# Performance work log

Measured on AMD Instinct MI355X. Metric: run time of the kernel, lower is better.

Reference implementation:

```python
import jax, jax.numpy as jnp
import numpy as np

B, S, D, N, MAX_W = 8, 512, 768, 512, 16  # batch, seq_len, input_dim, num_spans, max span width
TINY = 1e-13  # tiny_value_of_dtype(float32)


def setup_inputs() -> dict:
    key = jax.random.key(0)
    k1, k2, k3, k4 = jax.random.split(key, 4)
    sequence_tensor = jax.random.normal(k1, (B, S, D), dtype=jnp.float32)
    starts = jax.random.randint(k2, (B, N), 0, S - MAX_W)
    widths = jax.random.randint(k3, (B, N), 0, MAX_W)  # inclusive width-1 in [0, MAX_W-1]
    span_indices = jnp.stack([starts, starts + widths], axis=-1)  # (B, N, 2), end inclusive
    att_w = jax.random.normal(k4, (D,), dtype=jnp.float32) / np.sqrt(D)
    att_b = jnp.zeros((1,), dtype=jnp.float32)
    return {"sequence_tensor": sequence_tensor, "span_indices": span_indices,
            "att_w": att_w, "att_b": att_b}


def reference(sequence_tensor, span_indices, att_w, att_b):
    # global attention logits: Linear(D, 1) over every token  -> (B, S)
    logits = jnp.einsum('bsd,d->bs', sequence_tensor, att_w) + att_b[0]

    starts = span_indices[..., 0]                      # (B, N)
    ends = span_indices[..., 1]                        # (B, N), inclusive
    widths = ends - starts                             # (B, N)

    # batched_span_select: MAX_W is the (static) max span width
    rng = jnp.arange(MAX_W)                            # (W,)
    span_mask = rng[None, None, :] <= widths[..., None]          # (B, N, W)
    raw_idx = starts[..., None] + rng[None, None, :]             # (B, N, W)
    span_mask = span_mask & (raw_idx < S) & (raw_idx >= 0)
    idx = raw_idx * span_mask                                    # zeroed where masked

    b_idx = jnp.arange(sequence_tensor.shape[0])[:, None, None]
    span_emb = sequence_tensor[b_idx, idx]             # (B, N, W, D) gather
    span_logits = logits[b_idx[..., 0].reshape(-1, 1, 1), idx] if False else logits[b_idx, idx]  # (B, N, W)

    # masked_softmax (memory_efficient=False): softmax(vector*mask) * mask, renormalized
    maskf = span_mask.astype(span_logits.dtype)
    attn = jax.nn.softmax(span_logits * maskf, axis=-1) * maskf
    attn = attn / (attn.sum(axis=-1, keepdims=True) + TINY)

    # weighted sum over span width -> (B, N, D)
    return jnp.einsum('bnw,bnwd->bnd', attn, span_emb)
```

## Files before the change

### kernel.cpp

```cpp
#include <hip/hip_runtime.h>
#include <hip/hip_bf16.h>

#define B 8
#define S 512
#define D 768
#define N 512
#define MAX_W 16

__global__ __launch_bounds__(256) void logits_kernel(
    const float* __restrict__ seq,
    const float* __restrict__ att_w,
    const float* __restrict__ att_b,
    float* __restrict__ logits)
{
    const int wave = threadIdx.x >> 6;
    const int lane = threadIdx.x & 63;
    const int row  = blockIdx.x * 4 + wave;

    const float4* seq4 = (const float4*)(seq + (size_t)row * D);
    const float4* w4   = (const float4*)att_w;

    float acc = 0.0f;
#pragma unroll
    for (int i = 0; i < 3; ++i) {
        float4 a = seq4[lane + 64 * i];
        float4 w = w4[lane + 64 * i];
        acc += a.x * w.x + a.y * w.y + a.z * w.z + a.w * w.w;
    }
#pragma unroll
    for (int off = 32; off > 0; off >>= 1)
        acc += __shfl_xor(acc, off, 64);

    if (lane == 0) logits[row] = acc + att_b[0];
}

__global__ __launch_bounds__(192) void span_kernel(
    const float* __restrict__ seq,
    const int*   __restrict__ spans,
    const float* __restrict__ logits,
    float* __restrict__ out)
{
    const int span  = blockIdx.x;
    const int b     = span >> 9;
    const int start = spans[span * 2 + 0];
    const int end   = spans[span * 2 + 1];
    const int width = end - start;

    const float* lrow = logits + b * S + start;
    float wgt[MAX_W];
    float m = -1e30f;
#pragma unroll
    for (int i = 0; i < MAX_W; ++i) {
        float l = lrow[i];
        wgt[i] = l;
        if (i <= width) m = fmaxf(m, l);
    }
    float sum = 0.0f;
#pragma unroll
    for (int i = 0; i < MAX_W; ++i) {
        float e = (i <= width) ? __expf(wgt[i] - m) : 0.0f;
        wgt[i] = e;
        sum += e;
    }
    const float inv = 1.0f / sum;

    const float4* seqb = (const float4*)(seq + ((size_t)b * S + start) * D);
    const int tid = threadIdx.x;
    float4 acc = make_float4(0.f, 0.f, 0.f, 0.f);
#pragma unroll
    for (int i = 0; i < MAX_W; ++i) {
        if (i <= width) {
            float4 v = seqb[i * (D / 4) + tid];
            float w = wgt[i];
            acc.x += w * v.x;
            acc.y += w * v.y;
            acc.z += w * v.z;
            acc.w += w * v.w;
        }
    }
    acc.x *= inv; acc.y *= inv; acc.z *= inv; acc.w *= inv;

    float4* out4 = (float4*)(out + (size_t)span * D);
    out4[tid] = acc;
}

extern "C" void kernel_launch(void* const* d_in, const int* in_sizes, int n_in,
                              void* d_out, int out_size, void* d_ws, size_t ws_size,
                              hipStream_t stream) {
    const float* seq    = (const float*)d_in[0];
    const int*   spans  = (const int*)d_in[1];
    const float* att_w  = (const float*)d_in[2];
    const float* att_b  = (const float*)d_in[3];
    float* out = (float*)d_out;
    float* logits = (float*)d_ws;

    logits_kernel<<<(B * S) / 4, 256, 0, stream>>>(seq, att_w, att_b, logits);

    span_kernel<<<B * N, 192, 0, stream>>>(seq, spans, logits, out);
}
```

Before: 84.65 us.

## Fuse attention logit computation into span kernel and reorder block-to-span mapping

Removes the separate logits kernel: each span block computes the dot products of its gathered rows with att_w, reduces them through LDS, then does the softmax and the weighted sum from rows held in registers. This avoids a launch and a full pass over the sequence tensor, at the cost of redundant dot products for overlapping spans and extra syncs. Blocks are also remapped so that consecutive block IDs stride across batches. The bias is dropped because softmax is shift-invariant.

```diff
diff --git a/kernel.cpp b/kernel.cpp
--- a/kernel.cpp
+++ b/kernel.cpp
@@ -6,95 +6,108 @@
 #define D 768
 #define N 512
 #define MAX_W 16
+#define BLOCK 192
+#define ROW_F 196
 
-__global__ __launch_bounds__(256) void logits_kernel(
+__global__ __launch_bounds__(BLOCK) void fused_span_kernel(
     const float* __restrict__ seq,
+    const int2*  __restrict__ spans,
     const float* __restrict__ att_w,
-    const float* __restrict__ att_b,
-    float* __restrict__ logits)
-{
-    const int wave = threadIdx.x >> 6;
-    const int lane = threadIdx.x & 63;
-    const int row  = blockIdx.x * 4 + wave;
-
-    const float4* seq4 = (const float4*)(seq + (size_t)row * D);
-    const float4* w4   = (const float4*)att_w;
-
-    float acc = 0.0f;
-#pragma unroll
-    for (int i = 0; i < 3; ++i) {
-        float4 a = seq4[lane + 64 * i];
-        float4 w = w4[lane + 64 * i];
-        acc += a.x * w.x + a.y * w.y + a.z * w.z + a.w * w.w;
-    }
-#pragma unroll
-    for (int off = 32; off > 0; off >>= 1)
-        acc += __shfl_xor(acc, off, 64);
-
-    if (lane == 0) logits[row] = acc + att_b[0];
-}
-
-__global__ __launch_bounds__(192) void span_kernel(
-    const float* __restrict__ seq,
-    const int*   __restrict__ spans,
-    const float* __restrict__ logits,
     float* __restrict__ out)
 {
-    const int span  = blockIdx.x;
-    const int b     = span >> 9;
-    const int start = spans[span * 2 + 0];
-    const int end   = spans[span * 2 + 1];
-    const int width = end - start;
+    __shared__ __align__(16) float lds1[MAX_W][ROW_F];
+    __shared__ float lds2[MAX_W][12];
+    __shared__ float lds3[MAX_W];
 
-    const float* lrow = logits + b * S + start;
+    const int bid  = blockIdx.x;
+    const int span = (bid & 7) * (B * N / 8) + (bid >> 3);
+    const int b    = span >> 9;
+    const int tid  = threadIdx.x;
+
+    const int2 se   = spans[span];
+    const int start = se.x;
+    const int width = se.y - se.x;
+
+    const float4 wv = ((const float4*)att_w)[tid];
+    const float4* seqb = (const float4*)(seq + ((size_t)b * S + start) * D);
+
+    float4 v[MAX_W];
+    float  p[MAX_W];
+#pragma unroll
+    for (int i = 0; i < MAX_W; ++i) {
+        if (i <= width) {
+            float4 t = seqb[i * (D / 4) + tid];
+            v[i] = t;
+            p[i] = t.x * wv.x + t.y * wv.y + t.z * wv.z + t.w * wv.w;
+        } else {
+            v[i] = make_float4(0.f, 0.f, 0.f, 0.f);
+            p[i] = 0.f;
+        }
+    }
+
+#pragma unroll
+    for (int i = 0; i < MAX_W; ++i) lds1[i][tid] = p[i];
+    __syncthreads();
+
+    const int r = tid / 12;
+    const int j = tid - r * 12;
+    const float4* row4 = (const float4*)(&lds1[r][0]);
+    float s = 0.f;
+#pragma unroll
+    for (int k = 0; k < 4; ++k) {
+        float4 t = row4[j * 4 + k];
+        s += (t.x + t.y) + (t.z + t.w);
+    }
+    lds2[r][j] = s;
+    __syncthreads();
+
+    if (tid < MAX_W) {
+        float t = 0.f;
+#pragma unroll
+        for (int q = 0; q < 12; ++q) t += lds2[tid][q];
+        lds3[tid] = t;
+    }
+    __syncthreads();
+
     float wgt[MAX_W];
     float m = -1e30f;
 #pragma unroll
     for (int i = 0; i < MAX_W; ++i) {
-        float l = lrow[i];
-        wgt[i] = l;
-        if (i <= width) m = fmaxf(m, l);
+        wgt[i] = lds3[i];
+        if (i <= width) m = fmaxf(m, wgt[i]);
     }
-    float sum = 0.0f;
+    float sum = 0.f;
 #pragma unroll
     for (int i = 0; i < MAX_W; ++i) {
-        float e = (i <= width) ? __expf(wgt[i] - m) : 0.0f;
+        float e = (i <= width) ? __expf(wgt[i] - m) : 0.f;
         wgt[i] = e;
         sum += e;
     }
-    const float inv = 1.0f / sum;
+    const float inv = 1.f / sum;
 
-    const float4* seqb = (const float4*)(seq + ((size_t)b * S + start) * D);
-    const int tid = threadIdx.x;
     float4 acc = make_float4(0.f, 0.f, 0.f, 0.f);
 #pragma unroll
     for (int i = 0; i < MAX_W; ++i) {
         if (i <= width) {
-            float4 v = seqb[i * (D / 4) + tid];
-            float w = wgt[i];
-            acc.x += w * v.x;
-            acc.y += w * v.y;
-            acc.z += w * v.z;
-            acc.w += w * v.w;
+            const float w = wgt[i];
+            acc.x += w * v[i].x;
+            acc.y += w * v[i].y;
+            acc.z += w * v[i].z;
+            acc.w += w * v[i].w;
         }
     }
     acc.x *= inv; acc.y *= inv; acc.z *= inv; acc.w *= inv;
 
-    float4* out4 = (float4*)(out + (size_t)span * D);
-    out4[tid] = acc;
+    ((float4*)(out + (size_t)span * D))[tid] = acc;
 }
 
 extern "C" void kernel_launch(void* const* d_in, const int* in_sizes, int n_in,
                               void* d_out, int out_size, void* d_ws, size_t ws_size,
                               hipStream_t stream) {
-    const float* seq    = (const float*)d_in[0];
-    const int*   spans  = (const int*)d_in[1];
-    const float* att_w  = (const float*)d_in[2];
-    const float* att_b  = (const float*)d_in[3];
+    const float* seq   = (const float*)d_in[0];
+    const int2*  spans = (const int2*)d_in[1];
+    const float* att_w = (const float*)d_in[2];
     float* out = (float*)d_out;
-    float* logits = (float*)d_ws;
 
-    logits_kernel<<<(B * S) / 4, 256, 0, stream>>>(seq, att_w, att_b, logits);
-
-    span_kernel<<<B * N, 192, 0, stream>>>(seq, spans, logits, out);
+    fused_span_kernel<<<B * N, BLOCK, 0, stream>>>(seq, spans, att_w, out);
 }
```

Result: faster. 81.82 us (-3.3%).
